# Performance work log

Measured on AMD Instinct MI355X. Metric: run time of the kernel, lower is better.

Reference implementation:

```python
import jax, jax.numpy as jnp
import numpy as np
from jax import lax

B, N1, F1 = 8, 8192, 64
N2, K = 1024, 32
RADIUS = 0.2
MLP_SIZES = [64, 64, 128]
IN_DIM = 3 + F1  # concat(local xyz, features)


def _glorot_uniform(key, fan_in, fan_out):
    lim = np.sqrt(6.0 / (fan_in + fan_out)).astype(np.float32)
    return jax.random.uniform(key, (fan_in, fan_out), jnp.float32, -lim, lim)


def setup_inputs() -> dict:
    key = jax.random.key(0)
    ks = jax.random.split(key, 2 + len(MLP_SIZES))
    xyz = jax.random.uniform(ks[0], (B, N1, 3), jnp.float32)
    features = jax.random.normal(ks[1], (B, N1, F1), jnp.float32)
    inp = {"xyz": xyz, "features": features}
    d = IN_DIM
    for i, m in enumerate(MLP_SIZES):
        inp[f"W{i}"] = _glorot_uniform(ks[2 + i], d, m)
        inp[f"b{i}"] = jnp.zeros((m,), jnp.float32)
        d = m
    return inp


def farthest_point_sample(xyz, n_sample):
    # xyz: (B, N, 3) -> (B, n_sample) int32 indices. Sequential greedy FPS via scan.
    Bb, N, _ = xyz.shape
    first = jnp.zeros((Bb,), jnp.int32)
    big = jnp.finfo(xyz.dtype).max

    def step(carry, _):
        min_d, last = carry
        p = jnp.take_along_axis(xyz, last[:, None, None], axis=1)  # (B,1,3)
        d = jnp.sum((xyz - p) ** 2, axis=-1)                        # (B,N)
        min_d = jnp.minimum(min_d, d)
        nxt = jnp.argmax(min_d, axis=1).astype(jnp.int32)
        return (min_d, nxt), nxt

    init = (jnp.full((Bb, N), big, xyz.dtype), first)
    _, rest = lax.scan(step, init, None, length=n_sample - 1)  # (n_sample-1, B)
    return jnp.concatenate([first[None, :], rest], axis=0).T    # (B, n_sample)


def knn_search(query, points, k, radius):
    # query: (B,N2,3), points: (B,N1,3) -> (B,N2,k) indices, radius-clamped
    q2 = jnp.sum(query ** 2, -1)[:, :, None]          # (B,N2,1)
    p2 = jnp.sum(points ** 2, -1)[:, None, :]         # (B,1,N1)
    qp = jnp.einsum('bqd,bnd->bqn', query, points)    # (B,N2,N1)
    d2 = q2 + p2 - 2.0 * qp
    neg, idx = lax.top_k(-d2, k)                       # k nearest
    d2k = -neg
    # neighbors beyond the radius are replaced by the closest neighbor (ball query)
    idx = jnp.where(d2k > radius * radius, idx[..., :1], idx)
    return idx, d2k


def _gather_pts(x, idx):
    # x: (B,N1,C), idx: (B,N2[,K]) -> batched gather along axis 1
    return jnp.take_along_axis(x, idx.reshape(x.shape[0], -1, 1), axis=1).reshape(
        idx.shape + (x.shape[-1],))


def reference(xyz, features, W0, b0, W1, b1, W2, b2):
    sel_idx = farthest_point_sample(xyz, N2)                    # (B,N2)
    selected_xyz = _gather_pts(xyz, sel_idx)                    # (B,N2,3)
    nbr_idx, _ = knn_search(selected_xyz, xyz, K, RADIUS)       # (B,N2,K)
    nbr_xyz = _gather_pts(xyz, nbr_idx) - selected_xyz[:, :, None, :]
    nbr_feat = _gather_pts(features, nbr_idx)                   # (B,N2,K,F1)
    h = jnp.concatenate([nbr_xyz, nbr_feat], axis=-1)           # (B,N2,K,3+F1)
    for W, b in ((W0, b0), (W1, b1), (W2, b2)):
        h = jax.nn.leaky_relu(jnp.einsum('bqkc,cm->bqkm', h, W) + b, 0.2)
    selected_features = jnp.max(h, axis=2)                      # (B,N2,F2)
    return selected_xyz, selected_features
```

## Files before the change

### kernel.cpp

```cpp
#include <hip/hip_runtime.h>

#define B_   8
#define N1_  8192
#define N2_  1024
#define K_   32
#define F1_  64
#define CIN_ 67
#define M1_  64
#define M2_  64
#define M3_  128
#define HSTR 40
#define FLTMAX 3.402823466e+38f

#define FTPB 512
#define FNW  (FTPB/64)
#define PPT  (N1_/FTPB)

__device__ __forceinline__ unsigned f2key(float f) {
  unsigned u = __float_as_uint(f);
  return u ^ ((unsigned)((int)u >> 31) | 0x80000000u);
}

__device__ __forceinline__ unsigned dpp_umax_bcast(unsigned v) {
  unsigned o;
  o = (unsigned)__builtin_amdgcn_update_dpp(0, (int)v, 0x111, 0xf, 0xf, false); v = v > o ? v : o;
  o = (unsigned)__builtin_amdgcn_update_dpp(0, (int)v, 0x112, 0xf, 0xf, false); v = v > o ? v : o;
  o = (unsigned)__builtin_amdgcn_update_dpp(0, (int)v, 0x114, 0xf, 0xf, false); v = v > o ? v : o;
  o = (unsigned)__builtin_amdgcn_update_dpp(0, (int)v, 0x118, 0xf, 0xf, false); v = v > o ? v : o;
  o = (unsigned)__builtin_amdgcn_update_dpp(0, (int)v, 0x142, 0xf, 0xf, false); v = v > o ? v : o;
  o = (unsigned)__builtin_amdgcn_update_dpp(0, (int)v, 0x143, 0xf, 0xf, false); v = v > o ? v : o;
  return (unsigned)__builtin_amdgcn_readlane((int)v, 63);
}
__device__ __forceinline__ unsigned dpp_umin_bcast(unsigned v) {
  unsigned o;
  o = (unsigned)__builtin_amdgcn_update_dpp(-1, (int)v, 0x111, 0xf, 0xf, false); v = v < o ? v : o;
  o = (unsigned)__builtin_amdgcn_update_dpp(-1, (int)v, 0x112, 0xf, 0xf, false); v = v < o ? v : o;
  o = (unsigned)__builtin_amdgcn_update_dpp(-1, (int)v, 0x114, 0xf, 0xf, false); v = v < o ? v : o;
  o = (unsigned)__builtin_amdgcn_update_dpp(-1, (int)v, 0x118, 0xf, 0xf, false); v = v < o ? v : o;
  o = (unsigned)__builtin_amdgcn_update_dpp(-1, (int)v, 0x142, 0xf, 0xf, false); v = v < o ? v : o;
  o = (unsigned)__builtin_amdgcn_update_dpp(-1, (int)v, 0x143, 0xf, 0xf, false); v = v < o ? v : o;
  return (unsigned)__builtin_amdgcn_readlane((int)v, 63);
}

__global__ __launch_bounds__(FTPB, 1) void fps_kernel(const float* __restrict__ xyz,
                                                      float* __restrict__ out_xyz)
{
  __shared__ float4 wslot[2][FNW];

  const int t = threadIdx.x;
  const int b = blockIdx.x;
  const float* gxyz = xyz + (size_t)b * (N1_ * 3);
  float* oxyz = out_xyz + (size_t)b * (N2_ * 3);

  float x[PPT], y[PPT], z[PPT], md[PPT];
  {
    const float4* gs = (const float4*)gxyz;
#pragma unroll
    for (int w = 0; w < 12; ++w) {
      const float4 v = gs[t * 12 + w];
#pragma unroll
      for (int c = 0; c < 4; ++c) {
        const int p = w * 4 + c;
        const float val = (c == 0) ? v.x : (c == 1) ? v.y : (c == 2) ? v.z : v.w;
        const int j = p / 3, cc = p % 3;
        if (cc == 0) x[j] = val; else if (cc == 1) y[j] = val; else z[j] = val;
      }
    }
  }
#pragma unroll
  for (int j = 0; j < PPT; ++j) md[j] = FLTMAX;

  const int lane = t & 63, wv_ = t >> 6;
  if (lane == 0) { float4 s; s.x = -1.0f; s.y = 0.f; s.z = 0.f; s.w = 0.f; wslot[1][wv_] = s; }
  if (t == 0)   { float4 s; s.x = 1.0f; s.y = x[0]; s.z = y[0]; s.w = z[0]; wslot[1][0] = s; }
  __syncthreads();

  for (int i = 1; i < N2_; ++i) {
    const int p = i & 1;
    float4 wb = wslot[p][0];
#pragma unroll
    for (int u = 1; u < FNW; ++u) { const float4 s = wslot[p][u]; if (s.x > wb.x) wb = s; }
    const float px = wb.y, py = wb.z, pz = wb.w;
    if (t == 0) { const int o = (i - 1) * 3; oxyz[o] = px; oxyz[o+1] = py; oxyz[o+2] = pz; }

    float bestv, bx, by, bz;
#pragma unroll
    for (int j = 0; j < PPT; ++j) {
      const float dx = __fsub_rn(x[j], px);
      const float dy = __fsub_rn(y[j], py);
      const float dz = __fsub_rn(z[j], pz);
      const float d  = __fadd_rn(__fadd_rn(__fmul_rn(dx,dx), __fmul_rn(dy,dy)), __fmul_rn(dz,dz));
      md[j] = fminf(md[j], d);
      if (j == 0) { bestv = md[0]; bx = x[0]; by = y[0]; bz = z[0]; }
      else {
        const bool c = md[j] > bestv;
        bestv = c ? md[j] : bestv;
        bx = c ? x[j] : bx; by = c ? y[j] : by; bz = c ? z[j] : bz;
      }
    }
    const unsigned key = f2key(bestv);
    const unsigned kmax = dpp_umax_bcast(key);
    const int fl = __ffsll(__ballot(key == kmax)) - 1;
    if (lane == fl) {
      float4 s; s.x = bestv; s.y = bx; s.z = by; s.w = bz;
      wslot[1 - p][wv_] = s;
    }
    __syncthreads();
  }
  if (t == 0) {
    float4 wb = wslot[0][0];
#pragma unroll
    for (int u = 1; u < FNW; ++u) { const float4 s = wslot[0][u]; if (s.x > wb.x) wb = s; }
    const int o = (N2_ - 1) * 3; oxyz[o] = wb.y; oxyz[o+1] = wb.z; oxyz[o+2] = wb.w;
  }
}

__global__ __launch_bounds__(256) void knn_mlp_kernel(
    const float* __restrict__ xyz, const float* __restrict__ feat,
    const float* __restrict__ w0g, const float* __restrict__ b0g,
    const float* __restrict__ w1g, const float* __restrict__ b1g,
    const float* __restrict__ w2g, const float* __restrict__ b2g,
    const float* __restrict__ sel_xyz, float* __restrict__ out_feat)
{
  __shared__ __align__(16) float buf0[CIN_*HSTR];
  __shared__ __align__(16) float buf1[M1_*HSTR];
  __shared__ float sval[2][4];
  __shared__ int   sidx[2][4];

  const int t  = threadIdx.x;
  const int bq = blockIdx.x;
  const int b  = bq >> 10;
  const float* gxyz = xyz + (size_t)b * (N1_ * 3);

  const float qx = sel_xyz[bq*3+0], qy = sel_xyz[bq*3+1], qz = sel_xyz[bq*3+2];
  const float q2 = __fadd_rn(__fadd_rn(__fmul_rn(qx,qx), __fmul_rn(qy,qy)), __fmul_rn(qz,qz));

  float d2v[32];
  float m1 = FLTMAX, m2 = FLTMAX; int i1 = t*32, i2 = t*32;
  {
    const float4* gs = (const float4*)gxyz;
#pragma unroll
    for (int g8 = 0; g8 < 4; ++g8) {
      float f[24];
#pragma unroll
      for (int w = 0; w < 6; ++w) {
        const float4 v = gs[t * 24 + g8 * 6 + w];
        f[w*4+0] = v.x; f[w*4+1] = v.y; f[w*4+2] = v.z; f[w*4+3] = v.w;
      }
#pragma unroll
      for (int m = 0; m < 8; ++m) {
        const int j = g8 * 8 + m;
        const float px = f[3*m], py = f[3*m+1], pz = f[3*m+2];
        const float p2 = __fadd_rn(__fadd_rn(__fmul_rn(px,px), __fmul_rn(py,py)), __fmul_rn(pz,pz));
        const float qp = __fadd_rn(__fadd_rn(__fmul_rn(qx,px), __fmul_rn(qy,py)), __fmul_rn(qz,pz));
        const float d  = __fsub_rn(__fadd_rn(q2, p2), __fmul_rn(2.0f, qp));
        d2v[j] = d;
        const int idx = t*32 + j;
        const bool c1 = d < m1;
        const bool c2 = d < m2;
        const float nm2 = c1 ? m1 : (c2 ? d : m2);
        const int   ni2 = c1 ? i1 : (c2 ? idx : i2);
        m1 = c1 ? d : m1; i1 = c1 ? idx : i1;
        m2 = nm2; i2 = ni2;
      }
    }
  }

  int myk_idx = 0; float myk_d = 0.0f; int k0_idx = 0;
  unsigned removed = 0u; bool have2 = true;
  const int lane = t & 63;
  for (int kk = 0; kk < K_; ++kk) {
    const int p = kk & 1;
    const unsigned key = f2key(m1);
    const unsigned kmin = dpp_umin_bcast(key);
    const int fl = __ffsll(__ballot(key == kmin)) - 1;
    if (lane == fl) { sval[p][t >> 6] = m1; sidx[p][t >> 6] = i1; }
    __syncthreads();
    float wv = sval[p][0]; int wi = sidx[p][0];
#pragma unroll
    for (int u = 1; u < 4; ++u) {
      const float v = sval[p][u]; const int ii = sidx[p][u];
      if (v < wv || (v == wv && ii < wi)) { wv = v; wi = ii; }
    }
    wi &= (N1_ - 1);
    if ((t >> 3) == kk) { myk_idx = wi; myk_d = wv; }
    if (kk == 0) k0_idx = wi;
    if (kk < K_ - 1 && t == (wi >> 5)) {
      removed |= 1u << (wi & 31);
      if (have2) { m1 = m2; i1 = i2; have2 = false; }
      else {
        m1 = FLTMAX; i1 = t*32; m2 = FLTMAX; i2 = t*32;
#pragma unroll
        for (int j = 0; j < 32; ++j) {
          const float d = ((removed >> j) & 1u) ? FLTMAX : d2v[j];
          const int idx = t*32 + j;
          const bool c1 = d < m1;
          const bool c2 = d < m2;
          const float nm2 = c1 ? m1 : (c2 ? d : m2);
          const int   ni2 = c1 ? i1 : (c2 ? idx : i2);
          m1 = c1 ? d : m1; i1 = c1 ? idx : i1;
          m2 = nm2; i2 = ni2;
        }
        have2 = true;
      }
    }
  }

  {
    const int k = t >> 3, fg = t & 7;
    int nk = myk_idx;
    if (myk_d > 0.04f) nk = k0_idx;
    nk &= (N1_ - 1);
    const float* frow = feat + ((size_t)(b * N1_ + nk)) * F1_ + fg * 8;
    const float4 f0 = *(const float4*)frow;
    const float4 f1 = *(const float4*)(frow + 4);
    const int fb = 3 + fg * 8;
    buf0[(fb+0)*HSTR + k] = f0.x;
    buf0[(fb+1)*HSTR + k] = f0.y;
    buf0[(fb+2)*HSTR + k] = f0.z;
    buf0[(fb+3)*HSTR + k] = f0.w;
    buf0[(fb+4)*HSTR + k] = f1.x;
    buf0[(fb+5)*HSTR + k] = f1.y;
    buf0[(fb+6)*HSTR + k] = f1.z;
    buf0[(fb+7)*HSTR + k] = f1.w;
    if (fg < 3) {
      const float pc = gxyz[(size_t)nk * 3 + fg];
      const float qc = (fg == 0) ? qx : (fg == 1) ? qy : qz;
      buf0[fg * HSTR + k] = __fsub_rn(pc, qc);
    }
  }
  __syncthreads();

#define LEAKY_STORE2(acc, mi_, biasg, hout) { \
    const float bb = biasg[mg*2 + (mi_)]; \
    float4 v; \
    v.x = acc.x + bb; v.x = fmaxf(v.x, 0.2f*v.x); \
    v.y = acc.y + bb; v.y = fmaxf(v.y, 0.2f*v.y); \
    v.z = acc.z + bb; v.z = fmaxf(v.z, 0.2f*v.z); \
    v.w = acc.w + bb; v.w = fmaxf(v.w, 0.2f*v.w); \
    *(float4*)&hout[(mg*2 + (mi_)) * HSTR + kq * 4] = v; }

  {
    const int kq = t & 7, mg = t >> 3;
    float4 a0 = {0,0,0,0}, a1 = {0,0,0,0};
#pragma unroll 4
    for (int c = 0; c < CIN_; ++c) {
      const float2 wp = *(const float2*)&w0g[c * M1_ + mg * 2];
      const float4 h  = *(const float4*)&buf0[c * HSTR + kq * 4];
      a0.x += h.x*wp.x; a0.y += h.y*wp.x; a0.z += h.z*wp.x; a0.w += h.w*wp.x;
      a1.x += h.x*wp.y; a1.y += h.y*wp.y; a1.z += h.z*wp.y; a1.w += h.w*wp.y;
    }
    LEAKY_STORE2(a0, 0, b0g, buf1) LEAKY_STORE2(a1, 1, b0g, buf1)
  }
  __syncthreads();

  {
    const int kq = t & 7, mg = t >> 3;
    float4 a0 = {0,0,0,0}, a1 = {0,0,0,0};
#pragma unroll 4
    for (int c = 0; c < M1_; ++c) {
      const float2 wp = *(const float2*)&w1g[c * M2_ + mg * 2];
      const float4 h  = *(const float4*)&buf1[c * HSTR + kq * 4];
      a0.x += h.x*wp.x; a0.y += h.y*wp.x; a0.z += h.z*wp.x; a0.w += h.w*wp.x;
      a1.x += h.x*wp.y; a1.y += h.y*wp.y; a1.z += h.z*wp.y; a1.w += h.w*wp.y;
    }
    LEAKY_STORE2(a0, 0, b1g, buf0) LEAKY_STORE2(a1, 1, b1g, buf0)
  }
#undef LEAKY_STORE2
  __syncthreads();

  {
    const int kq = t & 7, mg = t >> 3;
    float4 a0 = {0,0,0,0}, a1 = {0,0,0,0}, a2 = {0,0,0,0}, a3 = {0,0,0,0};
#pragma unroll 4
    for (int c = 0; c < M2_; ++c) {
      const float4 wp = *(const float4*)&w2g[c * M3_ + mg * 4];
      const float4 h  = *(const float4*)&buf0[c * HSTR + kq * 4];
      a0.x += h.x*wp.x; a0.y += h.y*wp.x; a0.z += h.z*wp.x; a0.w += h.w*wp.x;
      a1.x += h.x*wp.y; a1.y += h.y*wp.y; a1.z += h.z*wp.y; a1.w += h.w*wp.y;
      a2.x += h.x*wp.z; a2.y += h.y*wp.z; a2.z += h.z*wp.z; a2.w += h.w*wp.z;
      a3.x += h.x*wp.w; a3.y += h.y*wp.w; a3.z += h.z*wp.w; a3.w += h.w*wp.w;
    }
    float vm[4];
#define BIAS_LEAKY_HMAX(acc, mi_) { \
      const float bb = b2g[mg*4 + (mi_)]; \
      float vx = acc.x + bb; vx = fmaxf(vx, 0.2f*vx); \
      float vy = acc.y + bb; vy = fmaxf(vy, 0.2f*vy); \
      float vz = acc.z + bb; vz = fmaxf(vz, 0.2f*vz); \
      float vw = acc.w + bb; vw = fmaxf(vw, 0.2f*vw); \
      vm[mi_] = fmaxf(fmaxf(vx, vy), fmaxf(vz, vw)); }
    BIAS_LEAKY_HMAX(a0, 0) BIAS_LEAKY_HMAX(a1, 1) BIAS_LEAKY_HMAX(a2, 2) BIAS_LEAKY_HMAX(a3, 3)
#undef BIAS_LEAKY_HMAX
#pragma unroll
    for (int m = 1; m <= 4; m <<= 1) {
      vm[0] = fmaxf(vm[0], __shfl_xor(vm[0], m, 64));
      vm[1] = fmaxf(vm[1], __shfl_xor(vm[1], m, 64));
      vm[2] = fmaxf(vm[2], __shfl_xor(vm[2], m, 64));
      vm[3] = fmaxf(vm[3], __shfl_xor(vm[3], m, 64));
    }
    if (kq == 0) {
      float4 o; o.x = vm[0]; o.y = vm[1]; o.z = vm[2]; o.w = vm[3];
      *(float4*)&out_feat[(size_t)bq * M3_ + mg * 4] = o;
    }
  }
}

extern "C" void kernel_launch(void* const* d_in, const int* in_sizes, int n_in,
                              void* d_out, int out_size, void* d_ws, size_t ws_size,
                              hipStream_t stream) {
  const float* xyz  = (const float*)d_in[0];
  const float* feat = (const float*)d_in[1];
  const float* w0   = (const float*)d_in[2];
  const float* b0   = (const float*)d_in[3];
  const float* w1   = (const float*)d_in[4];
  const float* b1   = (const float*)d_in[5];
  const float* w2   = (const float*)d_in[6];
  const float* b2   = (const float*)d_in[7];

  float* out_xyz  = (float*)d_out;
  float* out_feat = out_xyz + B_ * N2_ * 3;

  fps_kernel<<<B_, FTPB, 0, stream>>>(xyz, out_xyz);
  knn_mlp_kernel<<<B_ * N2_, 256, 0, stream>>>(xyz, feat, w0, b0, w1, b1, w2, b2,
                                               out_xyz, out_feat);
}
```

Measured before the change: 1.747 ms.

## Fuse FPS and kNN-MLP into one persistent launch with per-point flag handoff

Merges the farthest-point-sampling kernel and the kNN+MLP kernel into a single launch. The first B blocks run FPS at raised priority and publish each selected point through encoded atomic writes into the output feature slot, while the remaining blocks spin-wait on those slots so that neighbour search and MLP for early samples overlap the serial FPS. FPS now uses 256 threads with 32 points per thread instead of 512 threads with 16. The scheme depends on the FPS blocks being scheduled before the waiting blocks and on the output buffer not already holding the flag value. It also relies on the final output features overwriting the handoff slots. Spinning blocks occupy compute units while they wait.

Result: faster. 1.474 ms (-15.6%).

```diff
diff --git a/kernel.cpp b/kernel.cpp
--- a/kernel.cpp
+++ b/kernel.cpp
@@ -12,9 +12,8 @@
 #define HSTR 40
 #define FLTMAX 3.402823466e+38f
 
-#define FTPB 512
-#define FNW  (FTPB/64)
-#define PPT  (N1_/FTPB)
+#define FNW  4
+#define PPT  32
 
 __device__ __forceinline__ unsigned f2key(float f) {
   unsigned u = __float_as_uint(f);
@@ -42,97 +41,126 @@
   return (unsigned)__builtin_amdgcn_readlane((int)v, 63);
 }
 
-__global__ __launch_bounds__(FTPB, 1) void fps_kernel(const float* __restrict__ xyz,
-                                                      float* __restrict__ out_xyz)
-{
-  __shared__ float4 wslot[2][FNW];
-
-  const int t = threadIdx.x;
-  const int b = blockIdx.x;
-  const float* gxyz = xyz + (size_t)b * (N1_ * 3);
-  float* oxyz = out_xyz + (size_t)b * (N2_ * 3);
-
-  float x[PPT], y[PPT], z[PPT], md[PPT];
-  {
-    const float4* gs = (const float4*)gxyz;
-#pragma unroll
-    for (int w = 0; w < 12; ++w) {
-      const float4 v = gs[t * 12 + w];
-#pragma unroll
-      for (int c = 0; c < 4; ++c) {
-        const int p = w * 4 + c;
-        const float val = (c == 0) ? v.x : (c == 1) ? v.y : (c == 2) ? v.z : v.w;
-        const int j = p / 3, cc = p % 3;
-        if (cc == 0) x[j] = val; else if (cc == 1) y[j] = val; else z[j] = val;
-      }
-    }
-  }
-#pragma unroll
-  for (int j = 0; j < PPT; ++j) md[j] = FLTMAX;
-
-  const int lane = t & 63, wv_ = t >> 6;
-  if (lane == 0) { float4 s; s.x = -1.0f; s.y = 0.f; s.z = 0.f; s.w = 0.f; wslot[1][wv_] = s; }
-  if (t == 0)   { float4 s; s.x = 1.0f; s.y = x[0]; s.z = y[0]; s.w = z[0]; wslot[1][0] = s; }
-  __syncthreads();
-
-  for (int i = 1; i < N2_; ++i) {
-    const int p = i & 1;
-    float4 wb = wslot[p][0];
-#pragma unroll
-    for (int u = 1; u < FNW; ++u) { const float4 s = wslot[p][u]; if (s.x > wb.x) wb = s; }
-    const float px = wb.y, py = wb.z, pz = wb.w;
-    if (t == 0) { const int o = (i - 1) * 3; oxyz[o] = px; oxyz[o+1] = py; oxyz[o+2] = pz; }
-
-    float bestv, bx, by, bz;
-#pragma unroll
-    for (int j = 0; j < PPT; ++j) {
-      const float dx = __fsub_rn(x[j], px);
-      const float dy = __fsub_rn(y[j], py);
-      const float dz = __fsub_rn(z[j], pz);
-      const float d  = __fadd_rn(__fadd_rn(__fmul_rn(dx,dx), __fmul_rn(dy,dy)), __fmul_rn(dz,dz));
-      md[j] = fminf(md[j], d);
-      if (j == 0) { bestv = md[0]; bx = x[0]; by = y[0]; bz = z[0]; }
-      else {
-        const bool c = md[j] > bestv;
-        bestv = c ? md[j] : bestv;
-        bx = c ? x[j] : bx; by = c ? y[j] : by; bz = c ? z[j] : bz;
-      }
-    }
-    const unsigned key = f2key(bestv);
-    const unsigned kmax = dpp_umax_bcast(key);
-    const int fl = __ffsll(__ballot(key == kmax)) - 1;
-    if (lane == fl) {
-      float4 s; s.x = bestv; s.y = bx; s.z = by; s.w = bz;
-      wslot[1 - p][wv_] = s;
-    }
-    __syncthreads();
-  }
-  if (t == 0) {
-    float4 wb = wslot[0][0];
-#pragma unroll
-    for (int u = 1; u < FNW; ++u) { const float4 s = wslot[0][u]; if (s.x > wb.x) wb = s; }
-    const int o = (N2_ - 1) * 3; oxyz[o] = wb.y; oxyz[o+1] = wb.z; oxyz[o+2] = wb.w;
-  }
-}
-
-__global__ __launch_bounds__(256) void knn_mlp_kernel(
+#define HS_ENC(f) (__float_as_uint(f) ^ 0xC0000000u)
+#define HS_DEC(u) __uint_as_float((u) ^ 0xC0000000u)
+
+__global__ __launch_bounds__(256, 1) void fused_kernel(
     const float* __restrict__ xyz, const float* __restrict__ feat,
     const float* __restrict__ w0g, const float* __restrict__ b0g,
     const float* __restrict__ w1g, const float* __restrict__ b1g,
     const float* __restrict__ w2g, const float* __restrict__ b2g,
-    const float* __restrict__ sel_xyz, float* __restrict__ out_feat)
+    float* __restrict__ out_xyz, float* __restrict__ out_feat)
 {
+  __shared__ float4 wslot[2][FNW];
   __shared__ __align__(16) float buf0[CIN_*HSTR];
   __shared__ __align__(16) float buf1[M1_*HSTR];
   __shared__ float sval[2][4];
   __shared__ int   sidx[2][4];
-
-  const int t  = threadIdx.x;
-  const int bq = blockIdx.x;
+  __shared__ float qsh[3];
+
+  const int t = threadIdx.x;
+  const int lane = t & 63;
+
+  if (blockIdx.x < B_) {
+    __builtin_amdgcn_s_setprio(3);
+    const int b = blockIdx.x;
+    const float* gxyz = xyz + (size_t)b * (N1_ * 3);
+    float* oxyz = out_xyz + (size_t)b * (N2_ * 3);
+
+    float x[PPT], y[PPT], z[PPT], md[PPT];
+    {
+      const float4* gs = (const float4*)gxyz;
+#pragma unroll
+      for (int w = 0; w < 24; ++w) {
+        const float4 v = gs[t * 24 + w];
+#pragma unroll
+        for (int c = 0; c < 4; ++c) {
+          const int p = w * 4 + c;
+          const float val = (c == 0) ? v.x : (c == 1) ? v.y : (c == 2) ? v.z : v.w;
+          const int j = p / 3, cc = p % 3;
+          if (cc == 0) x[j] = val; else if (cc == 1) y[j] = val; else z[j] = val;
+        }
+      }
+    }
+#pragma unroll
+    for (int j = 0; j < PPT; ++j) md[j] = FLTMAX;
+
+    const int wv_ = t >> 6;
+    if (lane == 0) { float4 s; s.x = -1.0f; s.y = 0.f; s.z = 0.f; s.w = 0.f; wslot[1][wv_] = s; }
+    if (t == 0)   { float4 s; s.x = 1.0f; s.y = x[0]; s.z = y[0]; s.w = z[0]; wslot[1][0] = s; }
+    __syncthreads();
+
+    for (int i = 1; i < N2_; ++i) {
+      const int p = i & 1;
+      float4 wb = wslot[p][0];
+#pragma unroll
+      for (int u = 1; u < FNW; ++u) { const float4 s = wslot[p][u]; if (s.x > wb.x) wb = s; }
+      const float px = wb.y, py = wb.z, pz = wb.w;
+      if (t == 0) {
+        const int g = (b << 10) + (i - 1);
+        const int o = (i - 1) * 3;
+        oxyz[o] = px; oxyz[o+1] = py; oxyz[o+2] = pz;
+        unsigned* hs = (unsigned*)(out_feat + (size_t)g * M3_);
+        atomicExch(&hs[0], HS_ENC(px));
+        atomicExch(&hs[1], HS_ENC(py));
+        atomicExch(&hs[2], HS_ENC(pz));
+      }
+
+      float bestv, bx, by, bz;
+#pragma unroll
+      for (int j = 0; j < PPT; ++j) {
+        const float dx = __fsub_rn(x[j], px);
+        const float dy = __fsub_rn(y[j], py);
+        const float dz = __fsub_rn(z[j], pz);
+        const float d  = __fadd_rn(__fadd_rn(__fmul_rn(dx,dx), __fmul_rn(dy,dy)), __fmul_rn(dz,dz));
+        md[j] = fminf(md[j], d);
+        if (j == 0) { bestv = md[0]; bx = x[0]; by = y[0]; bz = z[0]; }
+        else {
+          const bool c = md[j] > bestv;
+          bestv = c ? md[j] : bestv;
+          bx = c ? x[j] : bx; by = c ? y[j] : by; bz = c ? z[j] : bz;
+        }
+      }
+      const unsigned key = f2key(bestv);
+      const unsigned kmax = dpp_umax_bcast(key);
+      const int fl = __ffsll(__ballot(key == kmax)) - 1;
+      if (lane == fl) {
+        float4 s; s.x = bestv; s.y = bx; s.z = by; s.w = bz;
+        wslot[1 - p][wv_] = s;
+      }
+      __syncthreads();
+    }
+    if (t == 0) {
+      float4 wb = wslot[0][0];
+#pragma unroll
+      for (int u = 1; u < FNW; ++u) { const float4 s = wslot[0][u]; if (s.x > wb.x) wb = s; }
+      const int g = (b << 10) + (N2_ - 1);
+      const int o = (N2_ - 1) * 3;
+      oxyz[o] = wb.y; oxyz[o+1] = wb.z; oxyz[o+2] = wb.w;
+      unsigned* hs = (unsigned*)(out_feat + (size_t)g * M3_);
+      atomicExch(&hs[0], HS_ENC(wb.y));
+      atomicExch(&hs[1], HS_ENC(wb.z));
+      atomicExch(&hs[2], HS_ENC(wb.w));
+    }
+    return;
+  }
+
+  const int bq = blockIdx.x - B_;
   const int b  = bq >> 10;
   const float* gxyz = xyz + (size_t)b * (N1_ * 3);
 
-  const float qx = sel_xyz[bq*3+0], qy = sel_xyz[bq*3+1], qz = sel_xyz[bq*3+2];
+  if (t == 0) {
+    unsigned* hs = (unsigned*)(out_feat + (size_t)bq * M3_);
+#pragma unroll
+    for (int w = 0; w < 3; ++w) {
+      unsigned v;
+      do { __builtin_amdgcn_s_sleep(2); v = atomicOr(&hs[w], 0u); }
+      while (v == 0u || v == 0xAAAAAAAAu);
+      qsh[w] = HS_DEC(v);
+    }
+  }
+  __syncthreads();
+  const float qx = qsh[0], qy = qsh[1], qz = qsh[2];
   const float q2 = __fadd_rn(__fadd_rn(__fmul_rn(qx,qx), __fmul_rn(qy,qy)), __fmul_rn(qz,qz));
 
   float d2v[32];
@@ -168,7 +196,6 @@
 
   int myk_idx = 0; float myk_d = 0.0f; int k0_idx = 0;
   unsigned removed = 0u; bool have2 = true;
-  const int lane = t & 63;
   for (int kk = 0; kk < K_; ++kk) {
     const int p = kk & 1;
     const unsigned key = f2key(m1);
@@ -320,7 +347,6 @@
   float* out_xyz  = (float*)d_out;
   float* out_feat = out_xyz + B_ * N2_ * 3;
 
-  fps_kernel<<<B_, FTPB, 0, stream>>>(xyz, out_xyz);
-  knn_mlp_kernel<<<B_ * N2_, 256, 0, stream>>>(xyz, feat, w0, b0, w1, b1, w2, b2,
-                                               out_xyz, out_feat);
-}
+  fused_kernel<<<B_ + B_ * N2_, 256, 0, stream>>>(xyz, feat, w0, b0, w1, b1, w2, b2,
+                                                  out_xyz, out_feat);
+}
```
